# Performance work log

Hardware: AMD Instinct MI355X
Metric: run time of the kernel (lower is better)

The kernel has to match this reference:

```python
import jax, jax.numpy as jnp
import numpy as np

B, S, H, NH = 8, 4096, 1024, 16
D = H // NH  # head dim = 64


def setup_inputs() -> dict:
    key = jax.random.key(0)
    k1, k2, k3, k4, k5 = jax.random.split(key, 5)
    hidden_states = jax.random.normal(k1, (B, S, H), dtype=jnp.float32)
    attention_mask = jnp.zeros((B, 1, 1, S), dtype=jnp.float32)
    # Linear params (torch convention: y = x @ W.T + b)
    Wq = jax.random.normal(k2, (H, H), dtype=jnp.float32) * 0.02
    bq = jnp.zeros((H,), dtype=jnp.float32)
    Wkv = jax.random.normal(k3, (H, H), dtype=jnp.float32) * 0.02
    bkv = jnp.zeros((H,), dtype=jnp.float32)
    return {"hidden_states": hidden_states, "attention_mask": attention_mask,
            "Wq": Wq, "bq": bq, "Wkv": Wkv, "bkv": bkv}


def reference(hidden_states, attention_mask, Wq, bq, Wkv, bkv):
    scale = 1.0 / jnp.sqrt(jnp.asarray(D, hidden_states.dtype))
    # projections; K and V share the same key_value projection
    q = hidden_states @ Wq.T + bq            # [B,S,H]
    kv = hidden_states @ Wkv.T + bkv         # [B,S,H]
    q = q.reshape(B, S, NH, D).transpose(0, 2, 1, 3)    # [B,h,S,d]
    k = kv.reshape(B, S, NH, D).transpose(0, 2, 1, 3)   # [B,h,S,d] (also V)

    # global token (position 0) attends to all positions
    gq = q[:, :, 0:1, :]                                 # [B,h,1,d]
    g_scores = jnp.einsum('bhqd,bhkd->bhqk', gq, k) * scale + attention_mask
    g_attn = jax.nn.softmax(g_scores, axis=-1)           # [B,h,1,S]
    g_vec = jnp.einsum('bhqk,bhkd->bhqd', g_attn, k)     # [B,h,1,d]

    # local tokens: each attends over 2 keys = {its own key, global vector}
    lq = q[:, :, 1:, :]                                  # [B,h,S-1,d]
    lk = k[:, :, 1:, :]                                  # [B,h,S-1,d]
    s_self = jnp.sum(lq * lk, axis=-1) * scale           # [B,h,S-1]
    s_glob = jnp.sum(lq * g_vec, axis=-1) * scale        # [B,h,S-1] (g_vec broadcasts)
    l_scores = jnp.stack([s_self, s_glob], axis=-1)      # [B,h,S-1,2]
    l_attn = jax.nn.softmax(l_scores, axis=-1)           # [B,h,S-1,2]
    l_vec = l_attn[..., 0:1] * lk + l_attn[..., 1:2] * g_vec  # [B,h,S-1,d]

    ctx = jnp.concatenate([g_vec, l_vec], axis=2)        # [B,h,S,d]
    ctx = ctx.transpose(0, 2, 1, 3).reshape(B, S, H)     # [B,S,H]
    local_attentions = l_attn[:, :, :, None, :]          # [B,h,S-1,1,2] as in torch
    return ctx, local_attentions
```

## Files before the change

kernel.cpp:

```cpp
#include <hip/hip_runtime.h>
#include <hip/hip_bf16.h>
#include <stdint.h>

#define NB 8
#define NS 4096
#define NHID 1024
#define NHEAD 16
#define ND 64
#define NCH 16
#define CHUNK 256
#define NT 16

typedef __attribute__((ext_vector_type(8))) __bf16 bf16x8;
typedef __attribute__((ext_vector_type(4))) __bf16 bf16x4;
typedef __attribute__((ext_vector_type(4))) float floatx4;

__device__ __forceinline__ void async_copy16(const __bf16* g, __bf16* l) {
  __builtin_amdgcn_global_load_lds(
      (const __attribute__((address_space(1))) void*)g,
      (__attribute__((address_space(3))) void*)l,
      16, 0, 0);
}

__global__ void cast_f32_to_bf16(const float* __restrict__ in,
                                 __bf16* __restrict__ out, int n) {
  int i = (blockIdx.x * blockDim.x + threadIdx.x) * 4;
  int stride = gridDim.x * blockDim.x * 4;
  for (; i < n; i += stride) {
    float4 v = *(const float4*)(in + i);
    bf16x4 o;
    o[0] = (__bf16)v.x; o[1] = (__bf16)v.y; o[2] = (__bf16)v.z; o[3] = (__bf16)v.w;
    *(bf16x4*)(out + i) = o;
  }
}


__device__ __forceinline__ void stage_half(const __bf16* __restrict__ G, int rb,
                                           int T, int kh, int matB,
                                           char* smem, int tid, int wid) {
  const uint32_t regionOff = (matB ? 65536u : 0u) + (uint32_t)(T & 1) * 32768u
                           + (uint32_t)kh * 16384u;
#pragma unroll
  for (int j = 0; j < 2; ++j) {
    uint32_t P = (uint32_t)(j * 512 + tid) * 16u;
    uint32_t L = P ^ (((P >> 7) & 3u) << 4);
    uint32_t r = L >> 6;
    uint32_t c = (L >> 4) & 3u;
    const __bf16* src = G + (size_t)(rb + (int)r) * 1024 + T * 64 + kh * 32 + (int)c * 8;
    async_copy16(src, (__bf16*)(smem + regionOff + (uint32_t)j * 8192u
                                + (uint32_t)wid * 1024u));
  }
}

__device__ __forceinline__ bf16x8 lds_frag(const char* smem, uint32_t base,
                                           int kk, int row, int hi4) {
  uint32_t Lrel = (uint32_t)kk * 16384u + (uint32_t)row * 64u + (uint32_t)hi4 * 16u;
  uint32_t phys = Lrel ^ (((Lrel >> 7) & 3u) << 4);
  return *(const bf16x8*)(smem + base + phys);
}

#define BARRIER asm volatile("s_barrier" ::: "memory")
#define WAIT_LGKM0 asm volatile("s_waitcnt lgkmcnt(0)" ::: "memory")
#define VM8 asm volatile("s_waitcnt vmcnt(8)" ::: "memory")
#define VM4 asm volatile("s_waitcnt vmcnt(4)" ::: "memory")
#define VM0 asm volatile("s_waitcnt vmcnt(0)" ::: "memory")

#define PHASE(KK, FMB, READB, STAGE_STMT, DRAIN_STMT)                          \
  do {                                                                         \
    if (READB) {                                                               \
      _Pragma("unroll")                                                        \
      for (int fn = 0; fn < 4; ++fn)                                           \
        bfrag[fn] = lds_frag(smem, 65536u + sl, KK, wn * 64 + fn * 16 + l15, hi4); \
    }                                                                          \
    _Pragma("unroll")                                                          \
    for (int fi = 0; fi < 4; ++fi)                                             \
      afrag[fi] = lds_frag(smem, sl, KK, wm * 128 + (FMB + fi) * 16 + l15, hi4); \
    STAGE_STMT;                                                                \
    BARRIER;                                                                   \
    WAIT_LGKM0;                                                                \
    __builtin_amdgcn_s_setprio(1);                                             \
    _Pragma("unroll")                                                          \
    for (int fi = 0; fi < 4; ++fi) {                                           \
      _Pragma("unroll")                                                        \
      for (int fn = 0; fn < 4; ++fn)                                           \
        acc[FMB + fi][fn] = __builtin_amdgcn_mfma_f32_16x16x32_bf16(           \
            afrag[fi], bfrag[fn], acc[FMB + fi][fn], 0, 0, 0);                 \
    }                                                                          \
    __builtin_amdgcn_s_setprio(0);                                             \
    DRAIN_STMT;                                                                \
    BARRIER;                                                                   \
  } while (0)

__global__ __launch_bounds__(512, 2) void gemm_qkv(
    const __bf16* __restrict__ A,
    const __bf16* __restrict__ W,
    const float* __restrict__ bq, const float* __restrict__ bkv,
    __bf16* __restrict__ Q, __bf16* __restrict__ KV) {
  __shared__ __align__(1024) char smem[131072];
  const int tid = threadIdx.x;
  const int lane = tid & 63;
  const int wid = tid >> 6;
  const int wm = wid >> 2;
  const int wn = wid & 3;
  const int l15 = lane & 15;
  const int hi4 = lane >> 4;

  const int bid = blockIdx.x;
  const int swz = ((bid & 7) << 7) | (bid >> 3);
  const int tn = swz & 7;
  const int tm = swz >> 3;
  const int rowBase = tm * 256;
  const int colBase = tn * 256;

  floatx4 acc[8][4];
#pragma unroll
  for (int m = 0; m < 8; m++)
#pragma unroll
    for (int n = 0; n < 4; n++)
#pragma unroll
      for (int j = 0; j < 4; j++) acc[m][n][j] = 0.f;

  stage_half(A, rowBase, 0, 0, 0, smem, tid, wid);
  stage_half(W, colBase, 0, 0, 1, smem, tid, wid);
  stage_half(A, rowBase, 0, 1, 0, smem, tid, wid);
  stage_half(W, colBase, 0, 1, 1, smem, tid, wid);
  stage_half(A, rowBase, 1, 0, 0, smem, tid, wid);
  stage_half(W, colBase, 1, 0, 1, smem, tid, wid);
  VM4;
  BARRIER;

  bf16x8 afrag[4], bfrag[4];
#pragma unroll 1
  for (int t = 0; t < NT; ++t) {
    const uint32_t sl = (uint32_t)(t & 1) * 32768u;
    PHASE(0, 0, 1,
          { if (t + 1 < NT) stage_half(A, rowBase, t + 1, 1, 0, smem, tid, wid); },
          ;);
    PHASE(0, 4, 0,
          { if (t + 1 < NT) stage_half(W, colBase, t + 1, 1, 1, smem, tid, wid); },
          { if (t < NT - 1) { VM8; } else { VM0; } });
    PHASE(1, 0, 1,
          { if (t + 2 < NT) stage_half(A, rowBase, t + 2, 0, 0, smem, tid, wid); },
          ;);
    PHASE(1, 4, 0,
          { if (t + 2 < NT) stage_half(W, colBase, t + 2, 0, 1, smem, tid, wid); },
          { if (t < NT - 2) { VM8; } else if (t == NT - 2) { VM4; } });
  }

  const bool isQ = (colBase < 1024);
  __bf16* __restrict__ dst = isQ ? Q : KV;
  const float* __restrict__ bias = isQ ? bq : bkv;
  const int colOff = isQ ? colBase : (colBase - 1024);
#pragma unroll
  for (int fm = 0; fm < 8; fm++) {
#pragma unroll
    for (int fn = 0; fn < 4; fn++) {
      const int col = colOff + wn * 64 + fn * 16 + l15;
      const float bv = bias[col];
#pragma unroll
      for (int j = 0; j < 4; j++) {
        const int row = rowBase + wm * 128 + fm * 16 + hi4 * 4 + j;
        dst[(size_t)row * 1024 + col] = (__bf16)(acc[fm][fn][j] + bv);
      }
    }
  }
}

__global__ __launch_bounds__(256) void global_attn_p1(
    const __bf16* __restrict__ Q, const __bf16* __restrict__ KV,
    const float* __restrict__ mask,
    float* __restrict__ pm, float* __restrict__ ps, float* __restrict__ pv) {
  __shared__ float gq[64];
  __shared__ float sc[CHUNK];
  __shared__ float red[256];
  const int bid = blockIdx.x;
  const int c = bid & (NCH - 1);
  const int h = (bid >> 4) & 15;
  const int b = bid >> 8;
  const int tid = threadIdx.x;
  const float scale = 0.125f;

  if (tid < 64) gq[tid] = (float)Q[(size_t)(b * NS) * NHID + h * 64 + tid];
  __syncthreads();

  const int s = c * CHUNK + tid;
  const __bf16* kr = KV + (size_t)(b * NS + s) * NHID + h * 64;
  float dot = 0.f;
#pragma unroll
  for (int d0 = 0; d0 < 64; d0 += 8) {
    bf16x8 kv8 = *(const bf16x8*)(kr + d0);
#pragma unroll
    for (int j = 0; j < 8; j++) dot += gq[d0 + j] * (float)kv8[j];
  }
  const float score = dot * scale + mask[b * NS + s];

  red[tid] = score; __syncthreads();
#pragma unroll
  for (int off = 128; off > 0; off >>= 1) {
    if (tid < off) red[tid] = fmaxf(red[tid], red[tid + off]);
    __syncthreads();
  }
  const float mc = red[0]; __syncthreads();

  const float p = __expf(score - mc);
  sc[tid] = p;
  red[tid] = p; __syncthreads();
#pragma unroll
  for (int off = 128; off > 0; off >>= 1) {
    if (tid < off) red[tid] += red[tid + off];
    __syncthreads();
  }
  const float sumc = red[0]; __syncthreads();

  const int d = tid & 63;
  const int g = tid >> 6;
  const __bf16* kcol = KV + (size_t)(b * NS + c * CHUNK + g * 64) * NHID + h * 64 + d;
  float acc = 0.f;
#pragma unroll 8
  for (int r = 0; r < 64; r++)
    acc += sc[g * 64 + r] * (float)kcol[(size_t)r * NHID];
  red[tid] = acc; __syncthreads();
  if (tid < 64) {
    pv[(size_t)bid * 64 + tid] = red[tid] + red[tid + 64] + red[tid + 128] + red[tid + 192];
    if (tid == 0) { pm[bid] = mc; ps[bid] = sumc; }
  }
}

__global__ __launch_bounds__(64) void global_attn_p2(
    const float* __restrict__ pm, const float* __restrict__ ps,
    const float* __restrict__ pv,
    float* __restrict__ gvec, float* __restrict__ ctx) {
  const int bh = blockIdx.x;
  const int lane = threadIdx.x;
  const int base = bh * NCH;
  float M = -1e30f;
#pragma unroll
  for (int c = 0; c < NCH; c++) M = fmaxf(M, pm[base + c]);
  float tot = 0.f, vec = 0.f;
#pragma unroll
  for (int c = 0; c < NCH; c++) {
    const float w = __expf(pm[base + c] - M);
    tot += ps[base + c] * w;
    vec += pv[(size_t)(base + c) * 64 + lane] * w;
  }
  const float gout = vec / tot;
  const int b = bh >> 4, h = bh & 15;
  gvec[bh * 64 + lane] = gout;
  ctx[(size_t)(b * NS) * NHID + h * 64 + lane] = gout;
}

__global__ __launch_bounds__(256) void local_attn(
    const __bf16* __restrict__ Q, const __bf16* __restrict__ KV,
    const float* __restrict__ gvec, float* __restrict__ ctx,
    float* __restrict__ lattn) {
  __shared__ float gs[NHEAD * 64];
  const int bb = blockIdx.x >> 10;
  const int s0 = (blockIdx.x & 1023) * 4;
  const int tid = threadIdx.x;
  for (int i = tid; i < NHEAD * 64; i += 256) gs[i] = gvec[bb * NHEAD * 64 + i];
  __syncthreads();
  const int wid = tid >> 6, lane = tid & 63;
  const int s = s0 + wid;
  if (s == 0) return;
  const int head = lane >> 2;
  const int dp = (lane & 3) * 16;
  const size_t rowoff = (size_t)(bb * NS + s) * NHID;
  const __bf16* qr = Q + rowoff + head * 64 + dp;
  const __bf16* kr = KV + rowoff + head * 64 + dp;
  float qv[16], kvv[16], gv[16];
  bf16x8 q0 = *(const bf16x8*)qr, q1 = *(const bf16x8*)(qr + 8);
  bf16x8 k0 = *(const bf16x8*)kr, k1 = *(const bf16x8*)(kr + 8);
#pragma unroll
  for (int j = 0; j < 8; j++) {
    qv[j] = (float)q0[j]; qv[j + 8] = (float)q1[j];
    kvv[j] = (float)k0[j]; kvv[j + 8] = (float)k1[j];
  }
#pragma unroll
  for (int j = 0; j < 16; j++) gv[j] = gs[head * 64 + dp + j];
  float sself = 0.f, sglob = 0.f;
#pragma unroll
  for (int j = 0; j < 16; j++) { sself += qv[j] * kvv[j]; sglob += qv[j] * gv[j]; }
  sself += __shfl_xor(sself, 1); sself += __shfl_xor(sself, 2);
  sglob += __shfl_xor(sglob, 1); sglob += __shfl_xor(sglob, 2);
  const float scale = 0.125f;
  sself *= scale; sglob *= scale;
  const float mm = fmaxf(sself, sglob);
  float p0 = __expf(sself - mm), p1 = __expf(sglob - mm);
  const float inv = 1.f / (p0 + p1);
  p0 *= inv; p1 *= inv;
  float* crow = ctx + rowoff + head * 64 + dp;
#pragma unroll
  for (int j4 = 0; j4 < 4; j4++) {
    float4 o;
    o.x = p0 * kvv[j4 * 4 + 0] + p1 * gv[j4 * 4 + 0];
    o.y = p0 * kvv[j4 * 4 + 1] + p1 * gv[j4 * 4 + 1];
    o.z = p0 * kvv[j4 * 4 + 2] + p1 * gv[j4 * 4 + 2];
    o.w = p0 * kvv[j4 * 4 + 3] + p1 * gv[j4 * 4 + 3];
    *(float4*)(crow + j4 * 4) = o;
  }
  if ((lane & 3) == 0) {
    const size_t li = ((size_t)(bb * NHEAD + head) * (NS - 1) + (s - 1)) * 2;
    lattn[li] = p0; lattn[li + 1] = p1;
  }
}

extern "C" void kernel_launch(void* const* d_in, const int* in_sizes, int n_in,
                              void* d_out, int out_size, void* d_ws, size_t ws_size,
                              hipStream_t stream) {
  const float* hs   = (const float*)d_in[0];
  const float* mask = (const float*)d_in[1];
  const float* Wq   = (const float*)d_in[2];
  const float* bq   = (const float*)d_in[3];
  const float* Wkv  = (const float*)d_in[4];
  const float* bkv  = (const float*)d_in[5];
  float* ctx   = (float*)d_out;
  float* lattn = ctx + (size_t)NB * NS * NHID;

  __bf16* hsb = (__bf16*)d_ws;
  __bf16* Wb  = hsb + (size_t)33554432;
  __bf16* Qb  = Wb  + (size_t)2097152;
  __bf16* KVb = Qb  + (size_t)33554432;
  float*  gvec = (float*)(KVb + (size_t)33554432);
  float*  pm   = gvec + 8192;
  float*  ps   = pm + 2048;
  float*  pv   = ps + 2048;

  cast_f32_to_bf16<<<4096, 256, 0, stream>>>(hs, hsb, 33554432);
  cast_f32_to_bf16<<<512, 256, 0, stream>>>(Wq, Wb, 1048576);
  cast_f32_to_bf16<<<512, 256, 0, stream>>>(Wkv, Wb + (size_t)1048576, 1048576);
  gemm_qkv<<<1024, 512, 0, stream>>>(hsb, Wb, bq, bkv, Qb, KVb);
  global_attn_p1<<<NB * NHEAD * NCH, 256, 0, stream>>>(Qb, KVb, mask, pm, ps, pv);
  global_attn_p2<<<NB * NHEAD, 64, 0, stream>>>(pm, ps, pv, gvec, ctx);
  local_attn<<<NB * (NS / 4), 256, 0, stream>>>(Qb, KVb, gvec, ctx, lattn);
}
```

Measured before the change: 461.4 us.

## Merge cast kernels, vectorize GEMM epilogue via swapped MFMA operands, batch local rows

Combines the three f32-to-bf16 cast launches into a single grid-stride kernel to cut launch overhead. Swaps the MFMA A/B operands so each lane holds four consecutive output columns, which lets the GEMM epilogue issue one 8-byte bf16x4 store with a float4 bias load instead of four scattered 2-byte stores. The local attention kernel now handles four rows per wave with fewer blocks, amortizing the shared-memory load of the global vector. The operand swap transposes the accumulator layout, and the epilogue indexing has to match it exactly.

```diff
diff --git a/kernel.cpp b/kernel.cpp
--- a/kernel.cpp
+++ b/kernel.cpp
@@ -22,15 +22,25 @@
       16, 0, 0);
 }
 
-__global__ void cast_f32_to_bf16(const float* __restrict__ in,
-                                 __bf16* __restrict__ out, int n) {
-  int i = (blockIdx.x * blockDim.x + threadIdx.x) * 4;
-  int stride = gridDim.x * blockDim.x * 4;
-  for (; i < n; i += stride) {
-    float4 v = *(const float4*)(in + i);
+__global__ void cast_all(const float* __restrict__ hs,
+                         const float* __restrict__ Wq,
+                         const float* __restrict__ Wkv,
+                         __bf16* __restrict__ hsb, __bf16* __restrict__ Wb) {
+  const int HS_N = 33554432, W_N = 1048576;
+  const int total4 = (HS_N + 2 * W_N) / 4;
+  int i4 = blockIdx.x * blockDim.x + threadIdx.x;
+  const int stride = gridDim.x * blockDim.x;
+  for (; i4 < total4; i4 += stride) {
+    const int i = i4 * 4;
+    const float* src;
+    __bf16* dst;
+    if (i < HS_N) { src = hs + i; dst = hsb + i; }
+    else if (i < HS_N + W_N) { src = Wq + (i - HS_N); dst = Wb + (i - HS_N); }
+    else { src = Wkv + (i - HS_N - W_N); dst = Wb + W_N + (i - HS_N - W_N); }
+    float4 v = *(const float4*)src;
     bf16x4 o;
     o[0] = (__bf16)v.x; o[1] = (__bf16)v.y; o[2] = (__bf16)v.z; o[3] = (__bf16)v.w;
-    *(bf16x4*)(out + i) = o;
+    *(bf16x4*)dst = o;
   }
 }
 
@@ -84,7 +94,7 @@
       _Pragma("unroll")                                                        \
       for (int fn = 0; fn < 4; ++fn)                                           \
         acc[FMB + fi][fn] = __builtin_amdgcn_mfma_f32_16x16x32_bf16(           \
-            afrag[fi], bfrag[fn], acc[FMB + fi][fn], 0, 0, 0);                 \
+            bfrag[fn], afrag[fi], acc[FMB + fi][fn], 0, 0, 0);                 \
     }                                                                          \
     __builtin_amdgcn_s_setprio(0);                                             \
     DRAIN_STMT;                                                                \
@@ -153,15 +163,18 @@
   const int colOff = isQ ? colBase : (colBase - 1024);
 #pragma unroll
   for (int fm = 0; fm < 8; fm++) {
+    const int row = rowBase + wm * 128 + fm * 16 + l15;
+    __bf16* rp = dst + (size_t)row * 1024;
 #pragma unroll
     for (int fn = 0; fn < 4; fn++) {
-      const int col = colOff + wn * 64 + fn * 16 + l15;
-      const float bv = bias[col];
-#pragma unroll
-      for (int j = 0; j < 4; j++) {
-        const int row = rowBase + wm * 128 + fm * 16 + hi4 * 4 + j;
-        dst[(size_t)row * 1024 + col] = (__bf16)(acc[fm][fn][j] + bv);
-      }
+      const int c0 = colOff + wn * 64 + fn * 16 + hi4 * 4;
+      const float4 bv = *(const float4*)&bias[c0];
+      bf16x4 o;
+      o[0] = (__bf16)(acc[fm][fn][0] + bv.x);
+      o[1] = (__bf16)(acc[fm][fn][1] + bv.y);
+      o[2] = (__bf16)(acc[fm][fn][2] + bv.z);
+      o[3] = (__bf16)(acc[fm][fn][3] + bv.w);
+      *(bf16x4*)(rp + c0) = o;
     }
   }
 }
@@ -254,53 +267,58 @@
     const float* __restrict__ gvec, float* __restrict__ ctx,
     float* __restrict__ lattn) {
   __shared__ float gs[NHEAD * 64];
-  const int bb = blockIdx.x >> 10;
-  const int s0 = (blockIdx.x & 1023) * 4;
+  const int bb = blockIdx.x >> 8;
+  const int chunk = blockIdx.x & 255;
   const int tid = threadIdx.x;
   for (int i = tid; i < NHEAD * 64; i += 256) gs[i] = gvec[bb * NHEAD * 64 + i];
   __syncthreads();
   const int wid = tid >> 6, lane = tid & 63;
-  const int s = s0 + wid;
-  if (s == 0) return;
   const int head = lane >> 2;
   const int dp = (lane & 3) * 16;
-  const size_t rowoff = (size_t)(bb * NS + s) * NHID;
-  const __bf16* qr = Q + rowoff + head * 64 + dp;
-  const __bf16* kr = KV + rowoff + head * 64 + dp;
-  float qv[16], kvv[16], gv[16];
-  bf16x8 q0 = *(const bf16x8*)qr, q1 = *(const bf16x8*)(qr + 8);
-  bf16x8 k0 = *(const bf16x8*)kr, k1 = *(const bf16x8*)(kr + 8);
-#pragma unroll
-  for (int j = 0; j < 8; j++) {
-    qv[j] = (float)q0[j]; qv[j + 8] = (float)q1[j];
-    kvv[j] = (float)k0[j]; kvv[j + 8] = (float)k1[j];
-  }
+  float gv[16];
 #pragma unroll
   for (int j = 0; j < 16; j++) gv[j] = gs[head * 64 + dp + j];
-  float sself = 0.f, sglob = 0.f;
-#pragma unroll
-  for (int j = 0; j < 16; j++) { sself += qv[j] * kvv[j]; sglob += qv[j] * gv[j]; }
-  sself += __shfl_xor(sself, 1); sself += __shfl_xor(sself, 2);
-  sglob += __shfl_xor(sglob, 1); sglob += __shfl_xor(sglob, 2);
+  const int sBase = chunk * 16 + wid * 4;
   const float scale = 0.125f;
-  sself *= scale; sglob *= scale;
-  const float mm = fmaxf(sself, sglob);
-  float p0 = __expf(sself - mm), p1 = __expf(sglob - mm);
-  const float inv = 1.f / (p0 + p1);
-  p0 *= inv; p1 *= inv;
-  float* crow = ctx + rowoff + head * 64 + dp;
-#pragma unroll
-  for (int j4 = 0; j4 < 4; j4++) {
-    float4 o;
-    o.x = p0 * kvv[j4 * 4 + 0] + p1 * gv[j4 * 4 + 0];
-    o.y = p0 * kvv[j4 * 4 + 1] + p1 * gv[j4 * 4 + 1];
-    o.z = p0 * kvv[j4 * 4 + 2] + p1 * gv[j4 * 4 + 2];
-    o.w = p0 * kvv[j4 * 4 + 3] + p1 * gv[j4 * 4 + 3];
-    *(float4*)(crow + j4 * 4) = o;
-  }
-  if ((lane & 3) == 0) {
-    const size_t li = ((size_t)(bb * NHEAD + head) * (NS - 1) + (s - 1)) * 2;
-    lattn[li] = p0; lattn[li + 1] = p1;
+#pragma unroll 2
+  for (int it = 0; it < 4; ++it) {
+    const int s = sBase + it;
+    if (s == 0) continue;
+    const size_t rowoff = (size_t)(bb * NS + s) * NHID;
+    const __bf16* qr = Q + rowoff + head * 64 + dp;
+    const __bf16* kr = KV + rowoff + head * 64 + dp;
+    float qv[16], kvv[16];
+    bf16x8 q0 = *(const bf16x8*)qr, q1 = *(const bf16x8*)(qr + 8);
+    bf16x8 k0 = *(const bf16x8*)kr, k1 = *(const bf16x8*)(kr + 8);
+#pragma unroll
+    for (int j = 0; j < 8; j++) {
+      qv[j] = (float)q0[j]; qv[j + 8] = (float)q1[j];
+      kvv[j] = (float)k0[j]; kvv[j + 8] = (float)k1[j];
+    }
+    float sself = 0.f, sglob = 0.f;
+#pragma unroll
+    for (int j = 0; j < 16; j++) { sself += qv[j] * kvv[j]; sglob += qv[j] * gv[j]; }
+    sself += __shfl_xor(sself, 1); sself += __shfl_xor(sself, 2);
+    sglob += __shfl_xor(sglob, 1); sglob += __shfl_xor(sglob, 2);
+    float s0 = sself * scale, s1 = sglob * scale;
+    const float mm = fmaxf(s0, s1);
+    float p0 = __expf(s0 - mm), p1 = __expf(s1 - mm);
+    const float inv = 1.f / (p0 + p1);
+    p0 *= inv; p1 *= inv;
+    float* crow = ctx + rowoff + head * 64 + dp;
+#pragma unroll
+    for (int j4 = 0; j4 < 4; j4++) {
+      float4 o;
+      o.x = p0 * kvv[j4 * 4 + 0] + p1 * gv[j4 * 4 + 0];
+      o.y = p0 * kvv[j4 * 4 + 1] + p1 * gv[j4 * 4 + 1];
+      o.z = p0 * kvv[j4 * 4 + 2] + p1 * gv[j4 * 4 + 2];
+      o.w = p0 * kvv[j4 * 4 + 3] + p1 * gv[j4 * 4 + 3];
+      *(float4*)(crow + j4 * 4) = o;
+    }
+    if ((lane & 3) == 0) {
+      const size_t li = ((size_t)(bb * NHEAD + head) * (NS - 1) + (s - 1)) * 2;
+      lattn[li] = p0; lattn[li + 1] = p1;
+    }
   }
 }
 
@@ -325,11 +343,9 @@
   float*  ps   = pm + 2048;
   float*  pv   = ps + 2048;
 
-  cast_f32_to_bf16<<<4096, 256, 0, stream>>>(hs, hsb, 33554432);
-  cast_f32_to_bf16<<<512, 256, 0, stream>>>(Wq, Wb, 1048576);
-  cast_f32_to_bf16<<<512, 256, 0, stream>>>(Wkv, Wb + (size_t)1048576, 1048576);
+  cast_all<<<4096, 256, 0, stream>>>(hs, Wq, Wkv, hsb, Wb);
   gemm_qkv<<<1024, 512, 0, stream>>>(hsb, Wb, bq, bkv, Qb, KVb);
   global_attn_p1<<<NB * NHEAD * NCH, 256, 0, stream>>>(Qb, KVb, mask, pm, ps, pv);
   global_attn_p2<<<NB * NHEAD, 64, 0, stream>>>(pm, ps, pv, gvec, ctx);
-  local_attn<<<NB * (NS / 4), 256, 0, stream>>>(Qb, KVb, gvec, ctx, lattn);
-}
+  local_attn<<<NB * 256, 256, 0, stream>>>(Qb, KVb, gvec, ctx, lattn);
+}
```

New measurement: 469.2 us. Within noise of the previous version (+1.7%).
